# Optimization experiments

Measured on AMD Instinct MI355X. Metric: run time of the kernel, lower is better.

The kernel has to match this reference:

```python
import jax, jax.numpy as jnp
import numpy as np

HEADS = 16
LN_EPS = 1e-6

def _layernorm(x, scale, bias):
    mu = jnp.mean(x, axis=-1, keepdims=True)
    var = jnp.mean(jnp.square(x - mu), axis=-1, keepdims=True)
    return (x - mu) * jax.lax.rsqrt(var + LN_EPS) * scale + bias

def setup_inputs() -> dict:
    key = jax.random.key(0)
    ks = jax.random.split(key, 5)
    B, L, D, F = 2, 2048, 1024, 4096
    s = lambda fan_in: 1.0 / np.sqrt(fan_in)
    return {
        'x': jax.random.normal(ks[0], (B, L, D), jnp.float32),
        'ln1_scale': jnp.ones((D,), jnp.float32),
        'ln1_bias': jnp.zeros((D,), jnp.float32),
        'w_qkv': jax.random.normal(ks[1], (D, 3 * D), jnp.float32) * s(D),
        'w_proj': jax.random.normal(ks[2], (D, D), jnp.float32) * s(D),
        'b_proj': jnp.zeros((D,), jnp.float32),
        'ln2_scale': jnp.ones((D,), jnp.float32),
        'ln2_bias': jnp.zeros((D,), jnp.float32),
        'w_mlp1': jax.random.normal(ks[3], (D, F), jnp.float32) * s(D),
        'b_mlp1': jnp.zeros((F,), jnp.float32),
        'w_mlp2': jax.random.normal(ks[4], (F, D), jnp.float32) * s(F),
        'b_mlp2': jnp.zeros((D,), jnp.float32),
    }

def reference(x, ln1_scale, ln1_bias, w_qkv, w_proj, b_proj,
              ln2_scale, ln2_bias, w_mlp1, b_mlp1, w_mlp2, b_mlp2):
    B, L, D = x.shape
    H = HEADS
    hd = D // H
    # pre-norm attention
    h = _layernorm(x, ln1_scale, ln1_bias)
    qkv = h @ w_qkv  # [B,L,3D]
    q, k, v = jnp.split(qkv, 3, axis=-1)
    q = q.reshape(B, L, H, hd).transpose(0, 2, 1, 3)  # [B,H,L,hd]
    k = k.reshape(B, L, H, hd).transpose(0, 2, 1, 3)
    v = v.reshape(B, L, H, hd).transpose(0, 2, 1, 3)
    scale = jnp.sqrt(jnp.float32(hd))
    scores = jnp.einsum('bhqd,bhkd->bhqk', q, k) / scale  # [B,H,L,L]
    attn = jax.nn.softmax(scores, axis=-1)
    out = jnp.einsum('bhqk,bhkd->bhqd', attn, v)  # [B,H,L,hd]
    out = out.transpose(0, 2, 1, 3).reshape(B, L, D)
    x = x + out @ w_proj + b_proj
    # pre-norm MLP
    h = _layernorm(x, ln2_scale, ln2_bias)
    m = jax.nn.gelu(h @ w_mlp1 + b_mlp1, approximate=True)
    return x + m @ w_mlp2 + b_mlp2
```

## Files before the change

kernel.cpp:

```cpp
#include <hip/hip_runtime.h>
#include <hip/hip_bf16.h>
#include <cstdint>
#include <cstddef>

typedef __bf16 bf16;
typedef __bf16 bf16x8 __attribute__((ext_vector_type(8)));
typedef float f32x4 __attribute__((ext_vector_type(4)));
typedef short short4v __attribute__((ext_vector_type(4)));
typedef unsigned uint2v __attribute__((ext_vector_type(2)));

#define GLB_AS(p) ((const __attribute__((address_space(1))) unsigned*)(unsigned long long)(p))
#define LDS_AS(p) ((__attribute__((address_space(3))) unsigned*)(unsigned)(unsigned long long)(p))

__device__ __forceinline__ void g2l16(const void* g, void* l) {
  __builtin_amdgcn_global_load_lds(GLB_AS(g), LDS_AS(l), 16, 0, 0);
}

__device__ __forceinline__ short f2bf(float x) {
  bf16 h = (bf16)x;
  return __builtin_bit_cast(short, h);
}

__device__ __forceinline__ unsigned pk_bf16(float a, float b) {
  __hip_bfloat162 h = __float22bfloat162_rn(float2{a, b});
  unsigned u;
  __builtin_memcpy(&u, &h, 4);
  return u;
}

extern "C" __device__ __attribute__((const)) float __ocml_native_exp2_f32(float);
extern "C" __device__ __attribute__((const)) float __ocml_native_recip_f32(float);
__device__ __forceinline__ float fast_exp2(float x) {
  return __ocml_native_exp2_f32(x);
}
__device__ __forceinline__ float fast_tanh(float a) {
  float e = __ocml_native_exp2_f32(a * 2.8853900817779268f);
  return 1.f - 2.f * __ocml_native_recip_f32(e + 1.f);
}

constexpr int MROWS = 4096;
constexpr size_t ATILE = (size_t)MROWS * 32;

#define QSCALE 0.18033688011112042f

__device__ __forceinline__ void transpose_body(
    const float* __restrict__ in, bf16* __restrict__ out, int K, int N,
    int bx, int by, float (*tile)[33], int tid)
{
  int tx = tid & 31, ty = tid >> 5;
  int n0 = bx * 32, k0 = by * 32;
  for (int i = ty; i < 32; i += 8)
    tile[i][tx] = in[(size_t)(k0 + i) * N + n0 + tx];
  __syncthreads();
  bf16* obase = out + (size_t)(k0 >> 5) * N * 32;
  for (int i = ty; i < 32; i += 8)
    obase[(size_t)(n0 + i) * 32 + tx] = (bf16)tile[tx][i];
}

__device__ __forceinline__ void ln_body(
    const float* __restrict__ x, const float* __restrict__ sc,
    const float* __restrict__ bi, bf16* __restrict__ out,
    int row, float* wsum, float* wsq, int tid)
{
  const float* xr = x + (size_t)row * 1024;
  int c = tid * 4;
  float4 xv = *(const float4*)(xr + c);
  float s = xv.x + xv.y + xv.z + xv.w;
  float q = xv.x * xv.x + xv.y * xv.y + xv.z * xv.z + xv.w * xv.w;
#pragma unroll
  for (int off = 1; off < 64; off <<= 1) {
    s += __shfl_xor(s, off);
    q += __shfl_xor(q, off);
  }
  int wv = tid >> 6;
  if ((tid & 63) == 0) { wsum[wv] = s; wsq[wv] = q; }
  __syncthreads();
  s = wsum[0] + wsum[1] + wsum[2] + wsum[3];
  q = wsq[0] + wsq[1] + wsq[2] + wsq[3];
  float mean = s * (1.f / 1024.f);
  float var = q * (1.f / 1024.f) - mean * mean;
  float rstd = rsqrtf(var + 1e-6f);
  float4 scv = *(const float4*)(sc + c);
  float4 biv = *(const float4*)(bi + c);
  bf16* o = out + (size_t)(c >> 5) * ATILE + (size_t)row * 32 + (c & 31);
  o[0] = (bf16)((xv.x - mean) * rstd * scv.x + biv.x);
  o[1] = (bf16)((xv.y - mean) * rstd * scv.y + biv.y);
  o[2] = (bf16)((xv.z - mean) * rstd * scv.z + biv.z);
  o[3] = (bf16)((xv.w - mean) * rstd * scv.w + biv.w);
}

__global__ __launch_bounds__(256) void prep_kernel(
    const float* __restrict__ wqkv, const float* __restrict__ wproj,
    const float* __restrict__ wmlp1, const float* __restrict__ wmlp2,
    bf16* __restrict__ wqkv_t, bf16* __restrict__ wproj_t,
    bf16* __restrict__ wmlp1_t, bf16* __restrict__ wmlp2_t,
    const float* __restrict__ x, const float* __restrict__ ln1s,
    const float* __restrict__ ln1b, bf16* __restrict__ hbuf)
{
  __shared__ float tile[32][33];
  __shared__ float wsum[4], wsq[4];
  int bid = blockIdx.x, tid = threadIdx.x;
  if (bid < 3072)
    transpose_body(wqkv, wqkv_t, 1024, 3072, bid % 96, bid / 96, tile, tid);
  else if (bid < 4096) {
    int i = bid - 3072;
    transpose_body(wproj, wproj_t, 1024, 1024, i % 32, i / 32, tile, tid);
  } else if (bid < 8192) {
    int i = bid - 4096;
    transpose_body(wmlp1, wmlp1_t, 1024, 4096, i % 128, i / 128, tile, tid);
  } else if (bid < 12288) {
    int i = bid - 8192;
    transpose_body(wmlp2, wmlp2_t, 4096, 1024, i % 32, i / 32, tile, tid);
  } else {
    ln_body(x, ln1s, ln1b, hbuf, bid - 12288, wsum, wsq, tid);
  }
}

__global__ __launch_bounds__(256) void ln_kernel(
    const float* __restrict__ x, const float* __restrict__ sc,
    const float* __restrict__ bi, bf16* __restrict__ out)
{
  __shared__ float wsum[4], wsq[4];
  ln_body(x, sc, bi, out, blockIdx.x, wsum, wsq, threadIdx.x);
}

template <int MT, int NT, int KS, int EPI>
__global__ __launch_bounds__(256) void gemm_tt(
    const bf16* __restrict__ A, const bf16* __restrict__ Bt,
    int N, int K,
    const float* __restrict__ bias, const float* __restrict__ resid,
    float* __restrict__ outf, bf16* __restrict__ ob0,
    bf16* __restrict__ ob1, bf16* __restrict__ ob2)
{
  constexpr int TM = MT * 32, TN = NT * 32;
  __shared__ __align__(16) bf16 As[2][TM * 32 * KS];
  __shared__ __align__(16) bf16 Bs[2][TN * 32 * KS];
  const int tid = threadIdx.x, lane = tid & 63, wave = tid >> 6;
  const int wm = wave >> 1, wn = wave & 1;
  const int quad = lane >> 4, l16 = lane & 15;

  int flat = blockIdx.x + gridDim.x * blockIdx.y;
  int xcd = flat & 7, rr = flat >> 3;
  int npx = gridDim.x >> 3;
  int bn = xcd * npx + (rr % npx);
  int bm = rr / npx;

  const size_t astride = ATILE;
  const size_t bstride = (size_t)N * 32;
  const bf16* Abase = A + (size_t)bm * TM * 32 + (size_t)lane * 8;
  const bf16* Bbase = Bt + (size_t)bn * TN * 32 + (size_t)lane * 8;

  f32x4 acc[MT][NT] = {};
  const int KT = K / (32 * KS);

  auto stage = [&](int buf, int kt) {
#pragma unroll
    for (int ks = 0; ks < KS; ks++) {
      const bf16* Ab = Abase + (size_t)(kt * KS + ks) * astride;
      const bf16* Bb = Bbase + (size_t)(kt * KS + ks) * bstride;
#pragma unroll
      for (int i = 0; i < MT / 2; i++)
        g2l16(Ab + (wave + 4 * i) * 512, &As[buf][ks * TM * 32 + (wave + 4 * i) * 512]);
#pragma unroll
      for (int i = 0; i < NT / 2; i++)
        g2l16(Bb + (wave + 4 * i) * 512, &Bs[buf][ks * TN * 32 + (wave + 4 * i) * 512]);
    }
  };

  stage(0, 0);
  int buf = 0;
  for (int kt = 0; kt < KT; kt++) {
    __syncthreads();
    if (kt + 1 < KT) stage(buf ^ 1, kt + 1);
#pragma unroll
    for (int kk = 0; kk < KS; kk++) {
      bf16x8 af[MT], bfr[NT];
#pragma unroll
      for (int mt = 0; mt < MT; mt++)
        af[mt] = *(const bf16x8*)&As[buf][kk * TM * 32 + (wm * MT * 16 + mt * 16 + l16) * 32 + quad * 8];
#pragma unroll
      for (int nt = 0; nt < NT; nt++)
        bfr[nt] = *(const bf16x8*)&Bs[buf][kk * TN * 32 + (wn * NT * 16 + nt * 16 + l16) * 32 + quad * 8];
#pragma unroll
      for (int mt = 0; mt < MT; mt++)
#pragma unroll
        for (int nt = 0; nt < NT; nt++)
          acc[mt][nt] = __builtin_amdgcn_mfma_f32_16x16x32_bf16(af[mt], bfr[nt], acc[mt][nt], 0, 0, 0);
    }
    buf ^= 1;
  }

#pragma unroll
  for (int mt = 0; mt < MT; mt++) {
#pragma unroll
    for (int nt = 0; nt < NT; nt++) {
      int row0 = bm * TM + wm * MT * 16 + mt * 16 + quad * 4;
      int col = bn * TN + wn * NT * 16 + nt * 16 + l16;
      if (EPI == 0) {
        int b = row0 >> 11, l = row0 & 2047;
        int which = col >> 10, d = col & 1023;
        int hh = d >> 6, hdi = d & 63;
        size_t bh = (size_t)(b * 16 + hh);
        if (which == 0) {
#pragma unroll
          for (int r = 0; r < 4; r++)
            ob0[(bh * 2048 + l + r) * 64 + hdi] = (bf16)(acc[mt][nt][r] * QSCALE);
        } else if (which == 1) {
#pragma unroll
          for (int r = 0; r < 4; r++)
            ob1[(bh * 2048 + l + r) * 64 + hdi] = (bf16)acc[mt][nt][r];
        } else {
          short4v v4;
#pragma unroll
          for (int r = 0; r < 4; r++) v4[r] = f2bf(acc[mt][nt][r]);
          *(short4v*)&ob2[(bh * 64 + hdi) * 2048 + l] = v4;
        }
      } else {
#pragma unroll
        for (int r = 0; r < 4; r++) {
          int row = row0 + r;
          float v = acc[mt][nt][r];
          if (EPI == 1) {
            size_t idx = (size_t)row * N + col;
            outf[idx] = v + bias[col] + resid[idx];
          } else {
            float t = v + bias[col];
            float a = 0.7978845608028654f * t * (1.f + 0.044715f * t * t);
            float g = 0.5f * t * (1.f + fast_tanh(a));
            ob0[(size_t)(col >> 5) * ATILE + (size_t)row * 32 + (col & 31)] = (bf16)g;
          }
        }
      }
    }
  }
}

__global__ __launch_bounds__(256, 2) void flash_attn(
    const bf16* __restrict__ Q, const bf16* __restrict__ Kg,
    const bf16* __restrict__ Vg, bf16* __restrict__ O)
{
  __shared__ __align__(16) bf16 Ks[128 * 64];
  __shared__ __align__(16) bf16 Vs[64 * 128];
  const int tid = threadIdx.x, lane = tid & 63, wave = tid >> 6;
  const int quad = lane >> 4, l16 = lane & 15;
  const int qt = blockIdx.x, bh = blockIdx.y;
  const int b = bh >> 4, h = bh & 15;

  const bf16* qg = Q + ((size_t)bh * 2048 + qt * 128) * 64;
  const bf16* kg = Kg + (size_t)bh * 2048 * 64;
  const bf16* vg = Vg + (size_t)bh * 64 * 2048;

  const int kw0 = ((tid >> 3) << 7) + (((tid & 7) << 4) ^ (((tid >> 3) & 7) << 4));
  const int vw0 = ((tid >> 4) << 8) + (((tid & 15) << 4) ^ (((tid >> 4) & 7) << 4));

  bf16x8 qf[2][2];
#pragma unroll
  for (int s = 0; s < 2; s++)
#pragma unroll
    for (int kk = 0; kk < 2; kk++)
      qf[s][kk] = *(const bf16x8*)&qg[(size_t)(wave * 32 + s * 16 + l16) * 64 + kk * 32 + quad * 8];

  f32x4 oacc[2][4] = {};
  float lrow[2] = {0.f, 0.f};

  bf16x8 kreg[4], vreg[4];
#pragma unroll
  for (int i = 0; i < 4; i++) {
    int t = tid + i * 256;
    kreg[i] = *(const bf16x8*)&kg[(size_t)(t >> 3) * 64 + (t & 7) * 8];
    vreg[i] = *(const bf16x8*)&vg[(size_t)(t >> 4) * 2048 + (t & 15) * 8];
  }

  for (int kt = 0; kt < 16; kt++) {
    __syncthreads();
#pragma unroll
    for (int i = 0; i < 4; i++) {
      *(bf16x8*)((char*)Ks + kw0 + i * 4096) = kreg[i];
      *(bf16x8*)((char*)Vs + vw0 + i * 4096) = vreg[i];
    }
    __syncthreads();
    if (kt < 15) {
#pragma unroll
      for (int i = 0; i < 4; i++) {
        int t = tid + i * 256;
        kreg[i] = *(const bf16x8*)&kg[((size_t)(kt + 1) * 128 + (t >> 3)) * 64 + (t & 7) * 8];
        vreg[i] = *(const bf16x8*)&vg[(size_t)(t >> 4) * 2048 + (kt + 1) * 128 + (t & 15) * 8];
      }
    }

    f32x4 sacc[2][8] = {};
#pragma unroll
    for (int kk = 0; kk < 2; kk++) {
#pragma unroll
      for (int ct = 0; ct < 8; ct++) {
        int krow = ct * 16 + l16;
        bf16x8 kf = *(const bf16x8*)((const char*)Ks + krow * 128 +
                                     ((kk * 64 + quad * 16) ^ ((l16 & 7) << 4)));
        sacc[0][ct] = __builtin_amdgcn_mfma_f32_16x16x32_bf16(kf, qf[0][kk], sacc[0][ct], 0, 0, 0);
        sacc[1][ct] = __builtin_amdgcn_mfma_f32_16x16x32_bf16(kf, qf[1][kk], sacc[1][ct], 0, 0, 0);
      }
    }

    short4v pf[2][8];
#pragma unroll
    for (int s = 0; s < 2; s++) {
      float sum = 0.f;
#pragma unroll
      for (int ct = 0; ct < 8; ct++) {
        float p0 = fast_exp2(sacc[s][ct][0]);
        float p1 = fast_exp2(sacc[s][ct][1]);
        float p2 = fast_exp2(sacc[s][ct][2]);
        float p3 = fast_exp2(sacc[s][ct][3]);
        sum += (p0 + p1) + (p2 + p3);
        uint2v u;
        u[0] = pk_bf16(p0, p1);
        u[1] = pk_bf16(p2, p3);
        pf[s][ct] = __builtin_bit_cast(short4v, u);
      }
      lrow[s] += sum;
    }

#pragma unroll
    for (int ot = 0; ot < 4; ot++) {
#pragma unroll
      for (int ct = 0; ct < 8; ct++) {
        int vrow = ot * 16 + l16;
        short4v vf = *(const short4v*)((const char*)Vs + vrow * 256 +
                                       ((ct * 32 + quad * 8) ^ ((l16 & 7) << 4)));
        oacc[0][ot] = __builtin_amdgcn_mfma_f32_16x16x16bf16_1k(vf, pf[0][ct], oacc[0][ot], 0, 0, 0);
        oacc[1][ot] = __builtin_amdgcn_mfma_f32_16x16x16bf16_1k(vf, pf[1][ct], oacc[1][ot], 0, 0, 0);
      }
    }
  }

#pragma unroll
  for (int s = 0; s < 2; s++) {
    float l = lrow[s];
    l += __shfl_xor(l, 16);
    l += __shfl_xor(l, 32);
    float inv = 1.f / l;
    int qrow = qt * 128 + wave * 32 + s * 16 + l16;
    size_t grow = (size_t)b * 2048 + qrow;
#pragma unroll
    for (int ot = 0; ot < 4; ot++) {
      int col = h * 64 + ot * 16 + quad * 4;
      short4v o4;
#pragma unroll
      for (int r = 0; r < 4; r++) o4[r] = f2bf(oacc[s][ot][r] * inv);
      *(short4v*)&O[(size_t)(col >> 5) * ATILE + grow * 32 + (col & 31)] = o4;
    }
  }
}

extern "C" void kernel_launch(void* const* d_in, const int* in_sizes, int n_in,
                              void* d_out, int out_size, void* d_ws, size_t ws_size,
                              hipStream_t stream)
{
  const float* x     = (const float*)d_in[0];
  const float* ln1s  = (const float*)d_in[1];
  const float* ln1b  = (const float*)d_in[2];
  const float* wqkv  = (const float*)d_in[3];
  const float* wproj = (const float*)d_in[4];
  const float* bproj = (const float*)d_in[5];
  const float* ln2s  = (const float*)d_in[6];
  const float* ln2b  = (const float*)d_in[7];
  const float* wmlp1 = (const float*)d_in[8];
  const float* bmlp1 = (const float*)d_in[9];
  const float* wmlp2 = (const float*)d_in[10];
  const float* bmlp2 = (const float*)d_in[11];
  float* out = (float*)d_out;

  char* ws = (char*)d_ws;
  bf16* wqkv_t  = (bf16*)(ws + 0);
  bf16* wproj_t = (bf16*)(ws + 6291456);
  bf16* wmlp1_t = (bf16*)(ws + 8388608);
  bf16* wmlp2_t = (bf16*)(ws + 16777216);
  bf16* hbuf    = (bf16*)(ws + 25165824);
  bf16* qb      = (bf16*)(ws + 33554432);
  bf16* kb      = (bf16*)(ws + 41943040);
  bf16* vb      = (bf16*)(ws + 50331648);
  bf16* aout    = (bf16*)(ws + 58720256);
  bf16* mbuf    = (bf16*)(ws + 33554432);

  prep_kernel<<<16384, 256, 0, stream>>>(wqkv, wproj, wmlp1, wmlp2,
                                         wqkv_t, wproj_t, wmlp1_t, wmlp2_t,
                                         x, ln1s, ln1b, hbuf);
  gemm_tt<4, 4, 1, 0><<<dim3(24, 32), 256, 0, stream>>>(hbuf, wqkv_t, 3072, 1024,
                                                        nullptr, nullptr, nullptr, qb, kb, vb);
  flash_attn<<<dim3(16, 32), 256, 0, stream>>>(qb, kb, vb, aout);
  gemm_tt<2, 4, 2, 1><<<dim3(8, 64), 256, 0, stream>>>(aout, wproj_t, 1024, 1024,
                                                       bproj, x, out, nullptr, nullptr, nullptr);
  ln_kernel<<<4096, 256, 0, stream>>>(out, ln2s, ln2b, hbuf);
  gemm_tt<4, 8, 1, 2><<<dim3(16, 32), 256, 0, stream>>>(hbuf, wmlp1_t, 4096, 1024,
                                                        bmlp1, nullptr, nullptr, mbuf, nullptr, nullptr);
  gemm_tt<2, 4, 2, 1><<<dim3(8, 64), 256, 0, stream>>>(mbuf, wmlp2_t, 1024, 4096,
                                                       bmlp2, out, out, nullptr, nullptr, nullptr);
}
```

Before: 333.0 us.

## Add triple-buffered LDS prefetch pipeline to QKV and MLP1 GEMMs

Adds a PF template parameter to the GEMM kernel. With PF=3 it keeps three LDS stages in flight and uses explicit vmcnt waits plus split barriers, so global-to-LDS loads for tile kt+2 are issued while tile kt is computed. This is meant to hide global load latency better than the previous double buffer. In exchange it uses more LDS per block, which may lower occupancy, and it depends on hand-counted vmcnt values.

```diff
diff --git a/kernel.cpp b/kernel.cpp
--- a/kernel.cpp
+++ b/kernel.cpp
@@ -124,7 +124,7 @@
   ln_body(x, sc, bi, out, blockIdx.x, wsum, wsq, threadIdx.x);
 }
 
-template <int MT, int NT, int KS, int EPI>
+template <int MT, int NT, int KS, int EPI, int PF>
 __global__ __launch_bounds__(256) void gemm_tt(
     const bf16* __restrict__ A, const bf16* __restrict__ Bt,
     int N, int K,
@@ -132,9 +132,10 @@
     float* __restrict__ outf, bf16* __restrict__ ob0,
     bf16* __restrict__ ob1, bf16* __restrict__ ob2)
 {
+  static_assert(PF == 2 || KS == 1, "PF3 path assumes KS==1");
   constexpr int TM = MT * 32, TN = NT * 32;
-  __shared__ __align__(16) bf16 As[2][TM * 32 * KS];
-  __shared__ __align__(16) bf16 Bs[2][TN * 32 * KS];
+  __shared__ __align__(16) bf16 As[PF][TM * 32 * KS];
+  __shared__ __align__(16) bf16 Bs[PF][TN * 32 * KS];
   const int tid = threadIdx.x, lane = tid & 63, wave = tid >> 6;
   const int wm = wave >> 1, wn = wave & 1;
   const int quad = lane >> 4, l16 = lane & 15;
@@ -167,27 +168,60 @@
     }
   };
 
-  stage(0, 0);
-  int buf = 0;
-  for (int kt = 0; kt < KT; kt++) {
-    __syncthreads();
-    if (kt + 1 < KT) stage(buf ^ 1, kt + 1);
-#pragma unroll
-    for (int kk = 0; kk < KS; kk++) {
+  if constexpr (PF == 2) {
+    stage(0, 0);
+    int buf = 0;
+    for (int kt = 0; kt < KT; kt++) {
+      __syncthreads();
+      if (kt + 1 < KT) stage(buf ^ 1, kt + 1);
+#pragma unroll
+      for (int kk = 0; kk < KS; kk++) {
+        bf16x8 af[MT], bfr[NT];
+#pragma unroll
+        for (int mt = 0; mt < MT; mt++)
+          af[mt] = *(const bf16x8*)&As[buf][kk * TM * 32 + (wm * MT * 16 + mt * 16 + l16) * 32 + quad * 8];
+#pragma unroll
+        for (int nt = 0; nt < NT; nt++)
+          bfr[nt] = *(const bf16x8*)&Bs[buf][kk * TN * 32 + (wn * NT * 16 + nt * 16 + l16) * 32 + quad * 8];
+#pragma unroll
+        for (int mt = 0; mt < MT; mt++)
+#pragma unroll
+          for (int nt = 0; nt < NT; nt++)
+            acc[mt][nt] = __builtin_amdgcn_mfma_f32_16x16x32_bf16(af[mt], bfr[nt], acc[mt][nt], 0, 0, 0);
+      }
+      buf ^= 1;
+    }
+  } else {
+    constexpr int STL = MT / 2 + NT / 2;
+    stage(0, 0);
+    stage(1, 1);
+    for (int kt = 0; kt < KT; kt++) {
+      if (kt + 1 < KT) {
+        if constexpr (STL == 6)      asm volatile("s_waitcnt vmcnt(6)" ::: "memory");
+        else if constexpr (STL == 4) asm volatile("s_waitcnt vmcnt(4)" ::: "memory");
+        else                         asm volatile("s_waitcnt vmcnt(3)" ::: "memory");
+      } else {
+        asm volatile("s_waitcnt vmcnt(0)" ::: "memory");
+      }
+      __builtin_amdgcn_s_barrier();
+      const int buf = kt % 3;
       bf16x8 af[MT], bfr[NT];
 #pragma unroll
       for (int mt = 0; mt < MT; mt++)
-        af[mt] = *(const bf16x8*)&As[buf][kk * TM * 32 + (wm * MT * 16 + mt * 16 + l16) * 32 + quad * 8];
+        af[mt] = *(const bf16x8*)&As[buf][(wm * MT * 16 + mt * 16 + l16) * 32 + quad * 8];
 #pragma unroll
       for (int nt = 0; nt < NT; nt++)
-        bfr[nt] = *(const bf16x8*)&Bs[buf][kk * TN * 32 + (wn * NT * 16 + nt * 16 + l16) * 32 + quad * 8];
+        bfr[nt] = *(const bf16x8*)&Bs[buf][(wn * NT * 16 + nt * 16 + l16) * 32 + quad * 8];
+      asm volatile("s_waitcnt lgkmcnt(0)" ::: "memory");
+      __builtin_amdgcn_sched_barrier(0);
+      __builtin_amdgcn_s_barrier();
+      if (kt + 2 < KT) stage((kt + 2) % 3, kt + 2);
 #pragma unroll
       for (int mt = 0; mt < MT; mt++)
 #pragma unroll
         for (int nt = 0; nt < NT; nt++)
           acc[mt][nt] = __builtin_amdgcn_mfma_f32_16x16x32_bf16(af[mt], bfr[nt], acc[mt][nt], 0, 0, 0);
     }
-    buf ^= 1;
   }
 
 #pragma unroll
@@ -385,14 +419,14 @@
   prep_kernel<<<16384, 256, 0, stream>>>(wqkv, wproj, wmlp1, wmlp2,
                                          wqkv_t, wproj_t, wmlp1_t, wmlp2_t,
                                          x, ln1s, ln1b, hbuf);
-  gemm_tt<4, 4, 1, 0><<<dim3(24, 32), 256, 0, stream>>>(hbuf, wqkv_t, 3072, 1024,
-                                                        nullptr, nullptr, nullptr, qb, kb, vb);
+  gemm_tt<4, 4, 1, 0, 3><<<dim3(24, 32), 256, 0, stream>>>(hbuf, wqkv_t, 3072, 1024,
+                                                           nullptr, nullptr, nullptr, qb, kb, vb);
   flash_attn<<<dim3(16, 32), 256, 0, stream>>>(qb, kb, vb, aout);
-  gemm_tt<2, 4, 2, 1><<<dim3(8, 64), 256, 0, stream>>>(aout, wproj_t, 1024, 1024,
-                                                       bproj, x, out, nullptr, nullptr, nullptr);
+  gemm_tt<2, 4, 2, 1, 2><<<dim3(8, 64), 256, 0, stream>>>(aout, wproj_t, 1024, 1024,
+                                                          bproj, x, out, nullptr, nullptr, nullptr);
   ln_kernel<<<4096, 256, 0, stream>>>(out, ln2s, ln2b, hbuf);
-  gemm_tt<4, 8, 1, 2><<<dim3(16, 32), 256, 0, stream>>>(hbuf, wmlp1_t, 4096, 1024,
-                                                        bmlp1, nullptr, nullptr, mbuf, nullptr, nullptr);
-  gemm_tt<2, 4, 2, 1><<<dim3(8, 64), 256, 0, stream>>>(mbuf, wmlp2_t, 1024, 4096,
-                                                       bmlp2, out, out, nullptr, nullptr, nullptr);
-}
+  gemm_tt<4, 8, 1, 2, 3><<<dim3(16, 32), 256, 0, stream>>>(hbuf, wmlp1_t, 4096, 1024,
+                                                           bmlp1, nullptr, nullptr, mbuf, nullptr, nullptr);
+  gemm_tt<2, 4, 2, 1, 2><<<dim3(8, 64), 256, 0, stream>>>(mbuf, wmlp2_t, 1024, 4096,
+                                                          bmlp2, out, out, nullptr, nullptr, nullptr);
+}
```

Measured after the change: 337.7 us. No clear change (+1.4%).

## Replace MLP1 GEMM with 8-wave 256x256 ping-pong pipelined GELU kernel

Applied to the files above, without the earlier changes.

Adds a dedicated 512-thread GEMM for the MLP up-projection. It uses 256x256 output tiles, double-buffered LDS filled by global_load_lds, and interleaves A/B prefetch with MFMA phases using barriers and s_setprio. It also remaps block indices so neighbouring N tiles land on the same XCD for L2 reuse. The goal is to hide load latency behind matrix math and raise arithmetic intensity, at the cost of more registers and LDS per block.

```diff
diff --git a/kernel.cpp b/kernel.cpp
--- a/kernel.cpp
+++ b/kernel.cpp
@@ -235,6 +235,145 @@
   }
 }
 
+__global__ __launch_bounds__(512, 2) void gemm8p_gelu(
+    const bf16* __restrict__ A, const bf16* __restrict__ Bt,
+    const float* __restrict__ bias, bf16* __restrict__ ob0)
+{
+  __shared__ __align__(16) bf16 As[4 * 8192];
+  __shared__ __align__(16) bf16 Bs[4 * 8192];
+  const int tid = threadIdx.x, lane = tid & 63, wave = tid >> 6;
+  const int quad = lane >> 4, l16 = lane & 15;
+  const int wm = wave >> 2, wn = wave & 3;
+
+  int flat = blockIdx.x + gridDim.x * blockIdx.y;
+  int xcd = flat & 7, rr = flat >> 3;
+  int bn = xcd * 2 + (rr & 1);
+  int bm = rr >> 1;
+
+  auto stA = [&](int buf, int ktile, int half) {
+    const bf16* g = A + (size_t)ktile * ATILE +
+                    ((size_t)bm * 256 + half * 128) * 32 + (size_t)tid * 8;
+    g2l16(g, &As[(buf * 2 + (ktile & 1)) * 8192 + half * 4096 + wave * 512]);
+  };
+  auto stB = [&](int buf, int ktile, int half) {
+    const bf16* g = Bt + (size_t)ktile * ATILE +
+                    ((size_t)bn * 256 + half * 128) * 32 + (size_t)tid * 8;
+    g2l16(g, &Bs[(buf * 2 + (ktile & 1)) * 8192 + half * 4096 + wave * 512]);
+  };
+
+  f32x4 acc[8][4] = {};
+  bf16x8 af[4][2], bfr[4][2];
+
+  stA(0, 0, 0); stA(0, 0, 1); stA(0, 1, 0); stA(0, 1, 1);
+  stB(0, 0, 0); stB(0, 0, 1); stB(0, 1, 0); stB(0, 1, 1);
+  asm volatile("s_waitcnt vmcnt(0)" ::: "memory");
+  __builtin_amdgcn_s_barrier();
+
+  for (int kt = 0; kt < 16; kt++) {
+    const int buf = kt & 1, nbuf = buf ^ 1;
+    const bool more = (kt + 1) < 16;
+    const int kA = (kt + 1) * 2;
+
+#pragma unroll
+    for (int mt = 0; mt < 4; mt++)
+#pragma unroll
+      for (int kk = 0; kk < 2; kk++)
+        af[mt][kk] = *(const bf16x8*)&As[(buf * 2 + kk) * 8192 +
+                       (wm * 128 + mt * 16 + l16) * 32 + quad * 8];
+#pragma unroll
+    for (int nt = 0; nt < 2; nt++)
+#pragma unroll
+      for (int kk = 0; kk < 2; kk++)
+        bfr[nt][kk] = *(const bf16x8*)&Bs[(buf * 2 + kk) * 8192 +
+                        (wn * 64 + nt * 16 + l16) * 32 + quad * 8];
+    if (more) { stA(nbuf, kA, 0); stA(nbuf, kA, 1); stA(nbuf, kA + 1, 0); stA(nbuf, kA + 1, 1); }
+    __builtin_amdgcn_s_barrier();
+    asm volatile("s_waitcnt lgkmcnt(0)" ::: "memory");
+    __builtin_amdgcn_sched_barrier(0);
+    __builtin_amdgcn_s_setprio(1);
+#pragma unroll
+    for (int mt = 0; mt < 4; mt++)
+#pragma unroll
+      for (int nt = 0; nt < 2; nt++)
+#pragma unroll
+        for (int kk = 0; kk < 2; kk++)
+          acc[mt][nt] = __builtin_amdgcn_mfma_f32_16x16x32_bf16(af[mt][kk], bfr[nt][kk], acc[mt][nt], 0, 0, 0);
+    __builtin_amdgcn_s_setprio(0);
+    __builtin_amdgcn_s_barrier();
+
+#pragma unroll
+    for (int nt = 2; nt < 4; nt++)
+#pragma unroll
+      for (int kk = 0; kk < 2; kk++)
+        bfr[nt][kk] = *(const bf16x8*)&Bs[(buf * 2 + kk) * 8192 +
+                        (wn * 64 + nt * 16 + l16) * 32 + quad * 8];
+    if (more) { stB(nbuf, kA, 0); stB(nbuf, kA, 1); stB(nbuf, kA + 1, 0); stB(nbuf, kA + 1, 1); }
+    __builtin_amdgcn_s_barrier();
+    asm volatile("s_waitcnt lgkmcnt(0)" ::: "memory");
+    __builtin_amdgcn_sched_barrier(0);
+    __builtin_amdgcn_s_setprio(1);
+#pragma unroll
+    for (int mt = 0; mt < 4; mt++)
+#pragma unroll
+      for (int nt = 2; nt < 4; nt++)
+#pragma unroll
+        for (int kk = 0; kk < 2; kk++)
+          acc[mt][nt] = __builtin_amdgcn_mfma_f32_16x16x32_bf16(af[mt][kk], bfr[nt][kk], acc[mt][nt], 0, 0, 0);
+    __builtin_amdgcn_s_setprio(0);
+    __builtin_amdgcn_s_barrier();
+
+#pragma unroll
+    for (int mt = 0; mt < 4; mt++)
+#pragma unroll
+      for (int kk = 0; kk < 2; kk++)
+        af[mt][kk] = *(const bf16x8*)&As[(buf * 2 + kk) * 8192 +
+                       (wm * 128 + (mt + 4) * 16 + l16) * 32 + quad * 8];
+    __builtin_amdgcn_s_barrier();
+    asm volatile("s_waitcnt lgkmcnt(0)" ::: "memory");
+    __builtin_amdgcn_sched_barrier(0);
+    __builtin_amdgcn_s_setprio(1);
+#pragma unroll
+    for (int mt = 0; mt < 4; mt++)
+#pragma unroll
+      for (int nt = 0; nt < 2; nt++)
+#pragma unroll
+        for (int kk = 0; kk < 2; kk++)
+          acc[mt + 4][nt] = __builtin_amdgcn_mfma_f32_16x16x32_bf16(af[mt][kk], bfr[nt][kk], acc[mt + 4][nt], 0, 0, 0);
+    __builtin_amdgcn_s_setprio(0);
+    __builtin_amdgcn_s_barrier();
+
+    __builtin_amdgcn_s_setprio(1);
+#pragma unroll
+    for (int mt = 0; mt < 4; mt++)
+#pragma unroll
+      for (int nt = 2; nt < 4; nt++)
+#pragma unroll
+        for (int kk = 0; kk < 2; kk++)
+          acc[mt + 4][nt] = __builtin_amdgcn_mfma_f32_16x16x32_bf16(af[mt][kk], bfr[nt][kk], acc[mt + 4][nt], 0, 0, 0);
+    __builtin_amdgcn_s_setprio(0);
+    asm volatile("s_waitcnt vmcnt(0)" ::: "memory");
+    __builtin_amdgcn_s_barrier();
+  }
+
+#pragma unroll
+  for (int mt = 0; mt < 8; mt++) {
+#pragma unroll
+    for (int nt = 0; nt < 4; nt++) {
+      int row0 = bm * 256 + wm * 128 + mt * 16 + quad * 4;
+      int col = bn * 256 + wn * 64 + nt * 16 + l16;
+      float bcol = bias[col];
+#pragma unroll
+      for (int r = 0; r < 4; r++) {
+        int row = row0 + r;
+        float t = acc[mt][nt][r] + bcol;
+        float a = 0.7978845608028654f * t * (1.f + 0.044715f * t * t);
+        float g = 0.5f * t * (1.f + fast_tanh(a));
+        ob0[(size_t)(col >> 5) * ATILE + (size_t)row * 32 + (col & 31)] = (bf16)g;
+      }
+    }
+  }
+}
+
 __global__ __launch_bounds__(256, 2) void flash_attn(
     const bf16* __restrict__ Q, const bf16* __restrict__ Kg,
     const bf16* __restrict__ Vg, bf16* __restrict__ O)
@@ -391,8 +530,7 @@
   gemm_tt<2, 4, 2, 1><<<dim3(8, 64), 256, 0, stream>>>(aout, wproj_t, 1024, 1024,
                                                        bproj, x, out, nullptr, nullptr, nullptr);
   ln_kernel<<<4096, 256, 0, stream>>>(out, ln2s, ln2b, hbuf);
-  gemm_tt<4, 8, 1, 2><<<dim3(16, 32), 256, 0, stream>>>(hbuf, wmlp1_t, 4096, 1024,
-                                                        bmlp1, nullptr, nullptr, mbuf, nullptr, nullptr);
+  gemm8p_gelu<<<dim3(16, 16), 512, 0, stream>>>(hbuf, wmlp1_t, bmlp1, mbuf);
   gemm_tt<2, 4, 2, 1><<<dim3(8, 64), 256, 0, stream>>>(mbuf, wmlp2_t, 1024, 4096,
                                                        bmlp2, out, out, nullptr, nullptr, nullptr);
 }
```

New measurement: 317.8 us. 1.05x faster.
